# Performance work log

Measured on AMD Instinct MI355X. Metric: run time of the kernel, lower is better.

Reference implementation:

```python
import jax, jax.numpy as jnp
import numpy as np
from jax import lax

# sign binarization to {-1,+1} with straight-through estimator (standard BNN binarizePM1)
@jax.custom_vjp
def binarize(x):
    return jnp.where(x >= 0, 1.0, -1.0).astype(x.dtype)

def _bin_fwd(x):
    return binarize(x), None

def _bin_bwd(_, g):
    return (g,)  # straight-through

binarize.defvjp(_bin_fwd, _bin_bwd)

def conv2d(x, w, b):
    # NCHW, OIHW, 3x3, stride 1, pad 1
    y = lax.conv_general_dilated(x, w, window_strides=(1, 1), padding=((1, 1), (1, 1)),
                                 dimension_numbers=('NCHW', 'OIHW', 'NCHW'))
    return y + b[None, :, None, None]

def maxpool2(x):
    return lax.reduce_window(x, -jnp.inf, lax.max, (1, 1, 2, 2), (1, 1, 2, 2), 'VALID')

def bn(x, gamma, beta, mean, var, eps=1e-5):
    # inference-mode batchnorm; broadcasts over channel axis 1 (4D) or feature axis 1 (2D)
    if x.ndim == 4:
        shp = (1, -1, 1, 1)
    else:
        shp = (1, -1)
    inv = gamma * lax.rsqrt(var + eps)
    return x * inv.reshape(shp) + (beta - mean * inv).reshape(shp)

def setup_inputs() -> dict:
    key = jax.random.key(0)
    ks = jax.random.split(key, 16)
    B = 4096
    d = {}
    d['x'] = jax.random.normal(ks[0], (B, 1, 28, 28), jnp.float32)
    d['conv1_w'] = jax.random.normal(ks[1], (64, 1, 3, 3), jnp.float32) * 0.1
    d['conv1_b'] = jax.random.normal(ks[2], (64,), jnp.float32) * 0.01
    d['conv2_w'] = jax.random.normal(ks[3], (64, 64, 3, 3), jnp.float32) * 0.05
    d['conv2_b'] = jax.random.normal(ks[4], (64,), jnp.float32) * 0.01
    d['fc1_w'] = jax.random.normal(ks[5], (2048, 7 * 7 * 64), jnp.float32) * 0.02
    d['fc1_b'] = jax.random.normal(ks[6], (2048,), jnp.float32) * 0.01
    d['fc2_w'] = jax.random.normal(ks[7], (10, 2048), jnp.float32) * 0.02
    d['fc2_b'] = jax.random.normal(ks[8], (10,), jnp.float32) * 0.01
    for i, (name, c) in enumerate([('bn1', 64), ('bn2', 64), ('bn3', 2048)]):
        d[name + '_gamma'] = jnp.ones((c,), jnp.float32)
        d[name + '_beta'] = jnp.zeros((c,), jnp.float32)
        d[name + '_mean'] = jax.random.normal(ks[9 + i], (c,), jnp.float32) * 0.1
        d[name + '_var'] = jax.random.uniform(ks[12 + i], (c,), jnp.float32, 0.5, 1.5)
    d['scale'] = jnp.array([1e-5], jnp.float32)
    return d

def reference(x, conv1_w, conv1_b, conv2_w, conv2_b, fc1_w, fc1_b, fc2_w, fc2_b,
              bn1_gamma, bn1_beta, bn1_mean, bn1_var,
              bn2_gamma, bn2_beta, bn2_mean, bn2_var,
              bn3_gamma, bn3_beta, bn3_mean, bn3_var, scale):
    h = conv2d(x, binarize(conv1_w), conv1_b)          # [B,64,28,28]
    h = maxpool2(h)                                    # [B,64,14,14]
    h = bn(h, bn1_gamma, bn1_beta, bn1_mean, bn1_var)
    h = jnp.clip(h, -1.0, 1.0)                         # hardtanh
    h = binarize(h)                                    # qact1
    h = conv2d(h, binarize(conv2_w), conv2_b)          # [B,64,14,14]
    h = maxpool2(h)                                    # [B,64,7,7]
    h = bn(h, bn2_gamma, bn2_beta, bn2_mean, bn2_var)
    h = jnp.clip(h, -1.0, 1.0)
    h = binarize(h)
    h = h.reshape(h.shape[0], -1)                      # [B,3136]
    h = h @ binarize(fc1_w).T + fc1_b                  # [B,2048]
    h = bn(h, bn3_gamma, bn3_beta, bn3_mean, bn3_var)
    h = jnp.clip(h, -1.0, 1.0)
    h = binarize(h)
    h = h @ binarize(fc2_w).T + fc2_b                  # [B,10]
    return h * scale
```

## Files before the change

### kernel.cpp

```cpp
#include <hip/hip_runtime.h>
#include <stdint.h>

typedef unsigned long long ULL;


__global__ void prep_sgn1(const float* __restrict__ w1, float* __restrict__ sgn1) {
    int t = blockIdx.x * 256 + threadIdx.x;
    if (t < 576) sgn1[t] = (w1[t] >= 0.f) ? 1.f : -1.f;
}

__global__ void prep_pack_small(const float* __restrict__ w2, const float* __restrict__ fc2w,
                                ULL* __restrict__ wb2, ULL* __restrict__ wbf2) {
    int wave = threadIdx.x >> 6, lane = threadIdx.x & 63;
    int W = blockIdx.x * 4 + wave;
    if (W < 576) {
        int co = W / 9, tap = W - co * 9;
        ULL wd = __ballot(w2[(co * 64 + lane) * 9 + tap] >= 0.f);
        if (lane == 0) wb2[W] = wd;
    } else if (W < 576 + 320) {
        int idx = W - 576;
        int n = idx >> 5, k = idx & 31;
        ULL wd = __ballot(fc2w[n * 2048 + k * 64 + lane] >= 0.f);
        if (lane == 0) wbf2[idx] = wd;
    }
}

__global__ void prep_pack_fc1(const float* __restrict__ fc1w, ULL* __restrict__ wbT) {
    int wave = threadIdx.x >> 6, lane = threadIdx.x & 63;
    int W = blockIdx.x * 4 + wave;
    int n = W >> 2, pq = W & 3;
    int p0 = pq * 13, p1 = (p0 + 13 < 49) ? p0 + 13 : 49;
    const float* row = fc1w + (size_t)n * 3136 + lane * 49;
    for (int p = p0; p < p1; ++p) {
        ULL wd = __ballot(row[p] >= 0.f);
        if (lane == 0) wbT[p * 2048 + n] = wd;
    }
}

__global__ __launch_bounds__(256) void k1_conv1(const float* __restrict__ x,
        const float* __restrict__ sgn1, const float* __restrict__ b1,
        const float* __restrict__ g, const float* __restrict__ be,
        const float* __restrict__ mu, const float* __restrict__ va,
        ULL* __restrict__ qact1) {
    __shared__ double invd[64], cd[64], bd[64];
    int b = blockIdx.x, t = threadIdx.x;
    if (t < 64) {
        double iv = (double)g[t] / sqrt((double)va[t] + 1e-5);
        invd[t] = iv;
        cd[t]  = (double)be[t] - (double)mu[t] * iv;
        bd[t]  = (double)b1[t];
    }
    __syncthreads();
    if (t < 196) {
        int py = t / 14, px = t - py * 14;
        int y0 = 2 * py - 1, x0 = 2 * px - 1;
        float patch[4][4];
        const float* xb = x + (size_t)b * 784;
        #pragma unroll
        for (int r = 0; r < 4; ++r) {
            int y = y0 + r;
            #pragma unroll
            for (int c = 0; c < 4; ++c) {
                int xx = x0 + c;
                patch[r][c] = (y >= 0 && y < 28 && xx >= 0 && xx < 28) ? xb[y * 28 + xx] : 0.f;
            }
        }
        ULL mask = 0;
        for (int co = 0; co < 64; ++co) {
            const float* s = sgn1 + co * 9;
            float a00 = 0.f, a01 = 0.f, a10 = 0.f, a11 = 0.f;
            #pragma unroll
            for (int ky = 0; ky < 3; ++ky) {
                #pragma unroll
                for (int kx = 0; kx < 3; ++kx) {
                    float sv = s[ky * 3 + kx];
                    a00 = fmaf(patch[ky][kx],         sv, a00);
                    a01 = fmaf(patch[ky][kx + 1],     sv, a01);
                    a10 = fmaf(patch[ky + 1][kx],     sv, a10);
                    a11 = fmaf(patch[ky + 1][kx + 1], sv, a11);
                }
            }
            float m = fmaxf(fmaxf(a00, a01), fmaxf(a10, a11));
            double v  = (double)m + bd[co];
            double tt = v * invd[co] + cd[co];
            mask |= (ULL)(tt >= 0.0) << co;
        }
        qact1[(size_t)b * 196 + t] = mask;
    }
}

__global__ __launch_bounds__(256) void k2_conv2(const ULL* __restrict__ qact1,
        const ULL* __restrict__ wb2, const float* __restrict__ b2,
        const float* __restrict__ g, const float* __restrict__ be,
        const float* __restrict__ mu, const float* __restrict__ va,
        ULL* __restrict__ qact2) {
    __shared__ ULL a_s[196];
    __shared__ ULL w_s[576];
    __shared__ double invd[64], cd[64], bd[64];
    int b = blockIdx.x, t = threadIdx.x;
    int wave = t >> 6, lane = t & 63;
    if (t < 196) a_s[t] = qact1[(size_t)b * 196 + t];
    for (int i = t; i < 576; i += 256) w_s[i] = wb2[i];
    if (t < 64) {
        double iv = (double)g[t] / sqrt((double)va[t] + 1e-5);
        invd[t] = iv;
        cd[t]  = (double)be[t] - (double)mu[t] * iv;
        bd[t]  = (double)b2[t];
    }
    __syncthreads();
    ULL wk[9];
    #pragma unroll
    for (int k = 0; k < 9; ++k) wk[k] = w_s[lane * 9 + k];
    for (int p = wave; p < 49; p += 4) {
        int py = p / 7, px = p - py * 7;
        int m = -1000000;
        #pragma unroll
        for (int dy = 0; dy < 2; ++dy) {
            #pragma unroll
            for (int dx = 0; dx < 2; ++dx) {
                int y = 2 * py + dy, xx = 2 * px + dx;
                int acc = 0;
                #pragma unroll
                for (int ky = 0; ky < 3; ++ky) {
                    int ny = y + ky - 1;
                    if (ny < 0 || ny >= 14) continue;
                    #pragma unroll
                    for (int kx = 0; kx < 3; ++kx) {
                        int nx = xx + kx - 1;
                        if (nx < 0 || nx >= 14) continue;
                        acc += 64 - 2 * (int)__popcll(a_s[ny * 14 + nx] ^ wk[ky * 3 + kx]);
                    }
                }
                m = max(m, acc);
            }
        }
        double v  = (double)m + bd[lane];
        double tt = v * invd[lane] + cd[lane];
        ULL word = __ballot(tt >= 0.0);
        if (lane == 0) qact2[(size_t)b * 49 + p] = word;
    }
}

__global__ __launch_bounds__(256) void k3_fc1(const ULL* __restrict__ qact2,
        const ULL* __restrict__ wbT, const float* __restrict__ fb,
        const float* __restrict__ g, const float* __restrict__ be,
        const float* __restrict__ mu, const float* __restrict__ va,
        ULL* __restrict__ hbits) {
    __shared__ ULL xs[784];
    int t = threadIdx.x, wave = t >> 6, lane = t & 63;
    int b0 = blockIdx.x * 16;
    int gidx = blockIdx.y * 4 + wave;
    int n = gidx * 64 + lane;
    for (int i = t; i < 784; i += 256) xs[i] = qact2[(size_t)b0 * 49 + i];
    double iv   = (double)g[n] / sqrt((double)va[n] + 1e-5);
    double cc   = (double)be[n] - (double)mu[n] * iv;
    double bias = (double)fb[n];
    __syncthreads();
    int acc[16];
    #pragma unroll
    for (int i = 0; i < 16; ++i) acc[i] = 0;
    for (int p = 0; p < 49; ++p) {
        ULL w = wbT[p * 2048 + n];
        #pragma unroll
        for (int i = 0; i < 16; ++i)
            acc[i] += (int)__popcll(xs[i * 49 + p] ^ w);
    }
    #pragma unroll
    for (int i = 0; i < 16; ++i) {
        int dot = 3136 - 2 * acc[i];
        double tt = ((double)dot + bias) * iv + cc;
        ULL word = __ballot(tt >= 0.0);
        if (lane == 0) hbits[(size_t)(b0 + i) * 32 + gidx] = word;
    }
}

__global__ __launch_bounds__(256) void k4_fc2(const ULL* __restrict__ hbits,
        const ULL* __restrict__ wbf2, const float* __restrict__ b2,
        const float* __restrict__ scale, float* __restrict__ out, int total) {
    int gid = blockIdx.x * 256 + threadIdx.x;
    if (gid >= total) return;
    int b = gid / 10, n = gid - b * 10;
    const ULL* h = hbits + (size_t)b * 32;
    const ULL* w = wbf2 + n * 32;
    int acc = 0;
    #pragma unroll
    for (int k = 0; k < 32; ++k) acc += (int)__popcll(h[k] ^ w[k]);
    int dot = 2048 - 2 * acc;
    double v = ((double)dot + (double)b2[n]) * (double)scale[0];
    out[gid] = (float)v;
}

extern "C" void kernel_launch(void* const* d_in, const int* in_sizes, int n_in,
                              void* d_out, int out_size, void* d_ws, size_t ws_size,
                              hipStream_t stream) {
    const float* x      = (const float*)d_in[0];
    const float* w1     = (const float*)d_in[1];
    const float* b1     = (const float*)d_in[2];
    const float* w2     = (const float*)d_in[3];
    const float* b2     = (const float*)d_in[4];
    const float* fc1w   = (const float*)d_in[5];
    const float* fc1b   = (const float*)d_in[6];
    const float* fc2w   = (const float*)d_in[7];
    const float* fc2b   = (const float*)d_in[8];
    const float* g1 = (const float*)d_in[9],  *be1 = (const float*)d_in[10],
               *mu1 = (const float*)d_in[11], *va1 = (const float*)d_in[12];
    const float* g2 = (const float*)d_in[13], *be2 = (const float*)d_in[14],
               *mu2 = (const float*)d_in[15], *va2 = (const float*)d_in[16];
    const float* g3 = (const float*)d_in[17], *be3 = (const float*)d_in[18],
               *mu3 = (const float*)d_in[19], *va3 = (const float*)d_in[20];
    const float* scale = (const float*)d_in[21];
    float* out = (float*)d_out;

    int B = in_sizes[0] / 784;

    char* ws = (char*)d_ws;
    ULL* qact1 = (ULL*)(ws);
    ULL* qact2 = (ULL*)(ws + (size_t)B * 196 * 8);
    ULL* hbits = (ULL*)(ws + (size_t)B * 245 * 8);
    char* wsw  = ws + (size_t)B * 277 * 8;
    ULL* wb2   = (ULL*)(wsw);
    ULL* wbT   = (ULL*)(wsw + 576 * 8);
    ULL* wbf2  = (ULL*)(wsw + 576 * 8 + 49 * 2048 * 8);
    float* sgn1 = (float*)(wsw + 576 * 8 + 49 * 2048 * 8 + 320 * 8);

    prep_sgn1<<<3, 256, 0, stream>>>(w1, sgn1);
    prep_pack_small<<<224, 256, 0, stream>>>(w2, fc2w, wb2, wbf2);
    prep_pack_fc1<<<2048, 256, 0, stream>>>(fc1w, wbT);

    k1_conv1<<<B, 256, 0, stream>>>(x, sgn1, b1, g1, be1, mu1, va1, qact1);
    k2_conv2<<<B, 256, 0, stream>>>(qact1, wb2, b2, g2, be2, mu2, va2, qact2);
    k3_fc1<<<dim3(B / 16, 8), 256, 0, stream>>>(qact2, wbT, fc1b, g3, be3, mu3, va3, hbits);
    int total = B * 10;
    k4_fc2<<<(total + 255) / 256, 256, 0, stream>>>(hbits, wbf2, fc2b, scale, out, total);
}
```

Before: 373.2 us.

## Restructure conv2 with padded tile, sliding register window and pad corrections

The binarized conv2 kernel now stores activations in a zero-padded 16x16 shared tile and uses 7 waves, one per pooled row. Each wave slides a 4x4 register window across the row, so branchy boundary checks are gone and each loaded input word is reused across neighbouring outputs. Zero padding is handled by precomputed per-channel correction terms. Per-channel BN constants are computed in registers instead of shared tables. Separately, the fc1 weight-packing prep kernel stages four rows in shared memory so the global reads are coalesced. The cost is more LDS per block for packing and more register pressure in conv2.

```diff
diff --git a/kernel.cpp b/kernel.cpp
--- a/kernel.cpp
+++ b/kernel.cpp
@@ -25,14 +25,18 @@
     }
 }
 
-__global__ void prep_pack_fc1(const float* __restrict__ fc1w, ULL* __restrict__ wbT) {
-    int wave = threadIdx.x >> 6, lane = threadIdx.x & 63;
-    int W = blockIdx.x * 4 + wave;
-    int n = W >> 2, pq = W & 3;
-    int p0 = pq * 13, p1 = (p0 + 13 < 49) ? p0 + 13 : 49;
-    const float* row = fc1w + (size_t)n * 3136 + lane * 49;
-    for (int p = p0; p < p1; ++p) {
-        ULL wd = __ballot(row[p] >= 0.f);
+__global__ __launch_bounds__(256) void prep_pack_fc1(const float* __restrict__ fc1w,
+                                                     ULL* __restrict__ wbT) {
+    __shared__ float rows[4 * 3136];
+    int t = threadIdx.x;
+    const float* src = fc1w + (size_t)blockIdx.x * 4 * 3136;
+    for (int i = t; i < 4 * 3136; i += 256) rows[i] = src[i];
+    __syncthreads();
+    int wave = t >> 6, lane = t & 63;
+    int n = blockIdx.x * 4 + wave;
+    const float* r = rows + wave * 3136 + lane * 49;
+    for (int p = 0; p < 49; ++p) {
+        ULL wd = __ballot(r[p] >= 0.f);
         if (lane == 0) wbT[p * 2048 + n] = wd;
     }
 }
@@ -89,55 +93,88 @@
     }
 }
 
-__global__ __launch_bounds__(256) void k2_conv2(const ULL* __restrict__ qact1,
+__global__ __launch_bounds__(448) void k2_conv2(const ULL* __restrict__ qact1,
         const ULL* __restrict__ wb2, const float* __restrict__ b2,
         const float* __restrict__ g, const float* __restrict__ be,
         const float* __restrict__ mu, const float* __restrict__ va,
         ULL* __restrict__ qact2) {
-    __shared__ ULL a_s[196];
-    __shared__ ULL w_s[576];
-    __shared__ double invd[64], cd[64], bd[64];
+    __shared__ ULL ap[16][16];
     int b = blockIdx.x, t = threadIdx.x;
-    int wave = t >> 6, lane = t & 63;
-    if (t < 196) a_s[t] = qact1[(size_t)b * 196 + t];
-    for (int i = t; i < 576; i += 256) w_s[i] = wb2[i];
-    if (t < 64) {
-        double iv = (double)g[t] / sqrt((double)va[t] + 1e-5);
-        invd[t] = iv;
-        cd[t]  = (double)be[t] - (double)mu[t] * iv;
-        bd[t]  = (double)b2[t];
-    }
-    __syncthreads();
+    int pr = t >> 6, lane = t & 63;
+    if (t < 256) ap[t >> 4][t & 15] = 0ULL;
+    __syncthreads();
+    if (t < 196) ap[1 + t / 14][1 + t % 14] = qact1[(size_t)b * 196 + t];
+
     ULL wk[9];
     #pragma unroll
-    for (int k = 0; k < 9; ++k) wk[k] = w_s[lane * 9 + k];
-    for (int p = wave; p < 49; p += 4) {
-        int py = p / 7, px = p - py * 7;
-        int m = -1000000;
-        #pragma unroll
-        for (int dy = 0; dy < 2; ++dy) {
-            #pragma unroll
-            for (int dx = 0; dx < 2; ++dx) {
-                int y = 2 * py + dy, xx = 2 * px + dx;
-                int acc = 0;
+    for (int k = 0; k < 9; ++k) wk[k] = wb2[lane * 9 + k];
+    int pw[9];
+    #pragma unroll
+    for (int k = 0; k < 9; ++k) pw[k] = 64 - 2 * (int)__popcll(wk[k]);
+    double iv   = (double)g[lane] / sqrt((double)va[lane] + 1e-5);
+    double cc   = (double)be[lane] - (double)mu[lane] * iv;
+    double bias = (double)b2[lane];
+
+    int corr[2][3];
+    #pragma unroll
+    for (int j = 0; j < 2; ++j) {
+        bool tpad = (pr == 0 && j == 0);
+        bool bpad = (pr == 6 && j == 1);
+        #pragma unroll
+        for (int cls = 0; cls < 3; ++cls) {
+            int cacc = 0;
+            #pragma unroll
+            for (int r = 0; r < 3; ++r) {
                 #pragma unroll
-                for (int ky = 0; ky < 3; ++ky) {
-                    int ny = y + ky - 1;
-                    if (ny < 0 || ny >= 14) continue;
-                    #pragma unroll
-                    for (int kx = 0; kx < 3; ++kx) {
-                        int nx = xx + kx - 1;
-                        if (nx < 0 || nx >= 14) continue;
-                        acc += 64 - 2 * (int)__popcll(a_s[ny * 14 + nx] ^ wk[ky * 3 + kx]);
-                    }
+                for (int k = 0; k < 3; ++k) {
+                    bool pad = (r == 0 && tpad) || (r == 2 && bpad) ||
+                               (k == 0 && cls == 0) || (k == 2 && cls == 2);
+                    if (pad) cacc += pw[r * 3 + k];
                 }
-                m = max(m, acc);
-            }
-        }
-        double v  = (double)m + bd[lane];
-        double tt = v * invd[lane] + cd[lane];
+            }
+            corr[j][cls] = cacc;
+        }
+    }
+    __syncthreads();
+
+    ULL win[4][4];
+    #pragma unroll
+    for (int r = 0; r < 4; ++r) {
+        win[r][0] = ap[2 * pr + r][0];
+        win[r][1] = ap[2 * pr + r][1];
+    }
+    for (int px = 0; px < 7; ++px) {
+        #pragma unroll
+        for (int r = 0; r < 4; ++r) {
+            win[r][2] = ap[2 * pr + r][2 * px + 2];
+            win[r][3] = ap[2 * pr + r][2 * px + 3];
+        }
+        int s00 = 0, s01 = 0, s10 = 0, s11 = 0;
+        #pragma unroll
+        for (int r = 0; r < 3; ++r) {
+            #pragma unroll
+            for (int k = 0; k < 3; ++k) {
+                ULL w = wk[r * 3 + k];
+                s00 += (int)__popcll(win[r][k]         ^ w);
+                s01 += (int)__popcll(win[r][k + 1]     ^ w);
+                s10 += (int)__popcll(win[r + 1][k]     ^ w);
+                s11 += (int)__popcll(win[r + 1][k + 1] ^ w);
+            }
+        }
+        int clsL = (px == 0) ? 0 : 1, clsR = (px == 6) ? 2 : 1;
+        int d00 = 576 - 2 * s00 - corr[0][clsL];
+        int d01 = 576 - 2 * s01 - corr[0][clsR];
+        int d10 = 576 - 2 * s10 - corr[1][clsL];
+        int d11 = 576 - 2 * s11 - corr[1][clsR];
+        int m = max(max(d00, d01), max(d10, d11));
+        double tt = ((double)m + bias) * iv + cc;
         ULL word = __ballot(tt >= 0.0);
-        if (lane == 0) qact2[(size_t)b * 49 + p] = word;
+        if (lane == 0) qact2[(size_t)b * 49 + pr * 7 + px] = word;
+        #pragma unroll
+        for (int r = 0; r < 4; ++r) {
+            win[r][0] = win[r][2];
+            win[r][1] = win[r][3];
+        }
     }
 }
 
@@ -225,10 +262,10 @@
 
     prep_sgn1<<<3, 256, 0, stream>>>(w1, sgn1);
     prep_pack_small<<<224, 256, 0, stream>>>(w2, fc2w, wb2, wbf2);
-    prep_pack_fc1<<<2048, 256, 0, stream>>>(fc1w, wbT);
+    prep_pack_fc1<<<512, 256, 0, stream>>>(fc1w, wbT);
 
     k1_conv1<<<B, 256, 0, stream>>>(x, sgn1, b1, g1, be1, mu1, va1, qact1);
-    k2_conv2<<<B, 256, 0, stream>>>(qact1, wb2, b2, g2, be2, mu2, va2, qact2);
+    k2_conv2<<<B, 448, 0, stream>>>(qact1, wb2, b2, g2, be2, mu2, va2, qact2);
     k3_fc1<<<dim3(B / 16, 8), 256, 0, stream>>>(qact2, wbT, fc1b, g3, be3, mu3, va3, hbits);
     int total = B * 10;
     k4_fc2<<<(total + 255) / 256, 256, 0, stream>>>(hbits, wbf2, fc2b, scale, out, total);
```

Result: faster. 339.1 us (-9.1%).
